# Performance work log

Measured on AMD Instinct MI355X. Metric: run time of the kernel, lower is better.

The kernel has to match this reference:

```python
import jax, jax.numpy as jnp
import numpy as np

N, E, F, H = 50000, 500000, 128, 128
EPS = 1e-5


def setup_inputs() -> dict:
    key = jax.random.key(0)
    ks = jax.random.split(key, 16)
    x = jax.random.normal(ks[0], (N, F), jnp.float32)
    edge_index = jax.random.randint(ks[1], (2, E), 0, N, dtype=jnp.int64)
    edge_weights = jax.random.uniform(ks[2], (E,), jnp.float32)
    def lin(k, fan_in, fan_out):
        s = 1.0 / np.sqrt(fan_in)
        return jax.random.uniform(k, (fan_out, fan_in), jnp.float32, -s, s)
    inp = {"x": x, "edge_index": edge_index, "edge_weights": edge_weights,
           "W1": lin(ks[3], F, H), "b1": jnp.zeros((H,), jnp.float32),
           "g1": jnp.ones((H,), jnp.float32), "be1": jnp.zeros((H,), jnp.float32),
           "W2": lin(ks[4], H, H), "b2": jnp.zeros((H,), jnp.float32),
           "g2": jnp.ones((H,), jnp.float32), "be2": jnp.zeros((H,), jnp.float32),
           "W3": lin(ks[5], H, H), "b3": jnp.zeros((H,), jnp.float32),
           "g3": jnp.ones((H,), jnp.float32), "be3": jnp.zeros((H,), jnp.float32)}
    return inp


def _gcn_conv(x, src, dst, ew, W, b):
    # PyG GCNConv: h = x @ W.T; add self loops (weight 1); symmetric norm; scatter-add; + bias
    n = x.shape[0]
    h = x @ W.T                                   # [n, H]
    loop = jnp.arange(n, dtype=src.dtype)
    s = jnp.concatenate([src, loop])
    d = jnp.concatenate([dst, loop])
    w = jnp.concatenate([ew, jnp.ones((n,), ew.dtype)])
    deg = jax.ops.segment_sum(w, d, num_segments=n)  # degree at target nodes
    safe = jnp.where(deg > 0, deg, 1.0)
    dinv = jnp.where(deg > 0, 1.0 / jnp.sqrt(safe), 0.0)
    norm = dinv[s] * w * dinv[d]                  # [E+n]
    msg = h[s] * norm[:, None]                    # gather + scale, [E+n, H]
    agg = jax.ops.segment_sum(msg, d, num_segments=n)
    return agg + b


def _bn(x, g, b):
    # BatchNorm1d in training mode: batch mean/var (biased) over nodes
    m = x.mean(axis=0)
    v = x.var(axis=0)
    return (x - m) * (g / jnp.sqrt(v + EPS)) + b


def reference(x, edge_index, edge_weights, W1, b1, g1, be1, W2, b2, g2, be2, W3, b3, g3, be3):
    src, dst = edge_index[0], edge_index[1]
    o = _bn(jax.nn.relu(_gcn_conv(x, src, dst, edge_weights, W1, b1)), g1, be1)
    o = _bn(jax.nn.relu(_gcn_conv(o, src, dst, edge_weights, W2, b2)), g2, be2)
    o = _bn(jax.nn.relu(_gcn_conv(o, src, dst, edge_weights, W3, b3)), g3, be3)
    return o
```

## Files before the change

### kernel.cpp

```cpp
#include <hip/hip_runtime.h>
#include <hip/hip_bf16.h>

#define HF 128
#define EPSV 1e-5f
#define PR 64
#define CAP 64

typedef __attribute__((ext_vector_type(8))) short short8;
typedef __attribute__((ext_vector_type(4))) float f32x4;

__device__ __forceinline__ short bf16bits(float f) {
    __hip_bfloat16 h = __float2bfloat16(f);
    return __builtin_bit_cast(short, h);
}


__global__ void fill_bucket(const int* __restrict__ src, const int* __restrict__ dst,
                            const float* __restrict__ w, int* __restrict__ cnt2,
                            int2* __restrict__ bucket, int E) {
    int e = blockIdx.x * 256 + threadIdx.x;
    if (e < E) {
        int d = dst[e];
        int pos = atomicAdd(&cnt2[d], 1);
        bucket[(d << 6) + pos] = make_int2(src[e], __float_as_int(w[e]));
    }
}

__global__ __launch_bounds__(256) void node_norm_pack(const int2* __restrict__ bucket,
                                                      const int* __restrict__ cnt2,
                                                      float* __restrict__ dinv,
                                                      float* __restrict__ ss,
                                                      const float* __restrict__ W1,
                                                      const float* __restrict__ W2,
                                                      const float* __restrict__ W3,
                                                      short* __restrict__ bf, int n) {
    int t = threadIdx.x;
    int wv = t >> 6, l = t & 63;
    int node = blockIdx.x * 4 + wv;
    if (node < n) {
        int c = cnt2[node];
        float v = 0.f;
        if (l < c) v = __int_as_float(bucket[(node << 6) + l].y);
        #pragma unroll
        for (int m = 32; m; m >>= 1) v += __shfl_xor(v, m);
        if (l == 0) dinv[node] = rsqrtf(1.0f + v);
    }
    if (blockIdx.x == 0) ss[t] = (t < 128) ? 1.0f : 0.0f;
    if (blockIdx.x < 24) {
        int tid = blockIdx.x * 256 + t;
        int L = tid >> 11;
        int r = tid & 2047;
        const float* W = (L == 0) ? W1 : (L == 1) ? W2 : W3;
        int ctg = r >> 8, ks = (r >> 6) & 3, ln = r & 63;
        int col = ctg * 16 + (ln & 15);
        int k0 = ks * 32 + (ln >> 4) * 8;
        const float* wrow = W + (size_t)col * HF + k0;
        short8 v;
        #pragma unroll
        for (int j = 0; j < 8; ++j) v[j] = bf16bits(wrow[j]);
        *(short8*)(bf + (size_t)tid * 8) = v;
    }
}


template<bool BF16SRC>
__global__ __launch_bounds__(256) void gemm_mfma(const void* __restrict__ Xv,
                                                 const short* __restrict__ bfrag,
                                                 const float* __restrict__ ss,
                                                 short* __restrict__ H, int n) {
    __shared__ __align__(16) char xl[64 * 256];
    int t = threadIdx.x;
    int r0 = blockIdx.x << 6;
    int w = t >> 6, l = t & 63;
    int cgw = w & 1, rgw = w >> 1;

    short8 bfr[4][4];
    #pragma unroll
    for (int ct = 0; ct < 4; ++ct)
        #pragma unroll
        for (int ks = 0; ks < 4; ++ks)
            bfr[ct][ks] = *(const short8*)(bfrag +
                (((size_t)((cgw * 4 + ct) * 4 + ks) * 64 + l) * 8));

    int pair = t & 15;
    const float4* ss4 = (const float4*)ss;
    float4 sca = ss4[pair * 2], scb = ss4[pair * 2 + 1];
    float4 sha = ss4[32 + pair * 2], shb = ss4[32 + pair * 2 + 1];
    #pragma unroll
    for (int it = 0; it < 4; ++it) {
        int row = (t >> 4) + it * 16;
        int rg = r0 + row; if (rg >= n) rg = n - 1;
        float f[8];
        if constexpr (BF16SRC) {
            const uint4* xp = (const uint4*)((const short*)Xv + (size_t)rg * HF);
            uint4 hv = xp[pair];
            f[0] = __uint_as_float(hv.x << 16); f[1] = __uint_as_float(hv.x & 0xFFFF0000u);
            f[2] = __uint_as_float(hv.y << 16); f[3] = __uint_as_float(hv.y & 0xFFFF0000u);
            f[4] = __uint_as_float(hv.z << 16); f[5] = __uint_as_float(hv.z & 0xFFFF0000u);
            f[6] = __uint_as_float(hv.w << 16); f[7] = __uint_as_float(hv.w & 0xFFFF0000u);
        } else {
            const float4* xp = (const float4*)((const float*)Xv + (size_t)rg * HF);
            float4 v0 = xp[2 * pair], v1 = xp[2 * pair + 1];
            f[0] = v0.x; f[1] = v0.y; f[2] = v0.z; f[3] = v0.w;
            f[4] = v1.x; f[5] = v1.y; f[6] = v1.z; f[7] = v1.w;
        }
        f[0] = fmaf(f[0], sca.x, sha.x); f[1] = fmaf(f[1], sca.y, sha.y);
        f[2] = fmaf(f[2], sca.z, sha.z); f[3] = fmaf(f[3], sca.w, sha.w);
        f[4] = fmaf(f[4], scb.x, shb.x); f[5] = fmaf(f[5], scb.y, shb.y);
        f[6] = fmaf(f[6], scb.z, shb.z); f[7] = fmaf(f[7], scb.w, shb.w);
        short8 s8;
        #pragma unroll
        for (int j = 0; j < 8; ++j) s8[j] = bf16bits(f[j]);
        int byte = row * 256 + pair * 16;
        byte ^= (row & 7) << 4;
        *(short8*)(xl + byte) = s8;
    }
    __syncthreads();

    f32x4 z = {0.f, 0.f, 0.f, 0.f};
    f32x4 acc[2][4];
    #pragma unroll
    for (int mt = 0; mt < 2; ++mt)
        #pragma unroll
        for (int ct = 0; ct < 4; ++ct) acc[mt][ct] = z;

    #pragma unroll
    for (int ks = 0; ks < 4; ++ks) {
        int kb = ks * 64 + (l >> 4) * 16;
        int row0 = rgw * 32 + (l & 15);
        int b0 = row0 * 256 + kb; b0 ^= (row0 & 7) << 4;
        int row1 = row0 + 16;
        int b1 = row1 * 256 + kb; b1 ^= (row1 & 7) << 4;
        short8 a0 = *(const short8*)(xl + b0);
        short8 a1 = *(const short8*)(xl + b1);
        #pragma unroll
        for (int ct = 0; ct < 4; ++ct) {
            acc[0][ct] = __builtin_amdgcn_mfma_f32_16x16x32_bf16(a0, bfr[ct][ks], acc[0][ct], 0, 0, 0);
            acc[1][ct] = __builtin_amdgcn_mfma_f32_16x16x32_bf16(a1, bfr[ct][ks], acc[1][ct], 0, 0, 0);
        }
    }

    #pragma unroll
    for (int mt = 0; mt < 2; ++mt) {
        int grow0 = r0 + rgw * 32 + mt * 16 + (l >> 4) * 4;
        #pragma unroll
        for (int reg = 0; reg < 4; ++reg) {
            int grow = grow0 + reg;
            if (grow < n) {
                short* hp = H + (size_t)grow * HF + cgw * 64 + (l & 15);
                #pragma unroll
                for (int ct = 0; ct < 4; ++ct) hp[ct * 16] = bf16bits(acc[mt][ct][reg]);
            }
        }
    }
}

__device__ __forceinline__ void bf2x_acc(unsigned u, float nv, float& a, float& b) {
    a = fmaf(__uint_as_float(u << 16), nv, a);
    b = fmaf(__uint_as_float(u & 0xFFFF0000u), nv, b);
}

__global__ __launch_bounds__(256) void agg_stats(const short* __restrict__ H,
                                                 const int* __restrict__ cnt2,
                                                 const int2* __restrict__ bucket,
                                                 const float* __restrict__ dinv,
                                                 const float* __restrict__ bias,
                                                 short* __restrict__ R,
                                                 float* __restrict__ partials, int n) {
    int t = threadIdx.x;
    int w = t >> 6, l = t & 63;
    int half = l >> 5, fl = l & 31;
    int node = (blockIdx.x << 3) + (w << 1) + half;
    float4 o = {0.f, 0.f, 0.f, 0.f};
    if (node < n) {
        float dv = dinv[node];
        uint2 hu = ((const uint2*)(H + (size_t)node * HF))[fl];
        float4 A, B = {0, 0, 0, 0}, C = {0, 0, 0, 0}, D = {0, 0, 0, 0};
        A.x = __uint_as_float(hu.x << 16) * dv;
        A.y = __uint_as_float(hu.x & 0xFFFF0000u) * dv;
        A.z = __uint_as_float(hu.y << 16) * dv;
        A.w = __uint_as_float(hu.y & 0xFFFF0000u) * dv;
        int beg = node << 6, end = beg + cnt2[node];
        int j = beg;
        for (; j + 4 <= end; j += 4) {
            int2 e0 = bucket[j], e1 = bucket[j + 1], e2 = bucket[j + 2], e3 = bucket[j + 3];
            float n0 = dinv[e0.x] * __int_as_float(e0.y);
            float n1 = dinv[e1.x] * __int_as_float(e1.y);
            float n2 = dinv[e2.x] * __int_as_float(e2.y);
            float n3 = dinv[e3.x] * __int_as_float(e3.y);
            uint2 u0 = ((const uint2*)(H + (size_t)e0.x * HF))[fl];
            uint2 u1 = ((const uint2*)(H + (size_t)e1.x * HF))[fl];
            uint2 u2 = ((const uint2*)(H + (size_t)e2.x * HF))[fl];
            uint2 u3 = ((const uint2*)(H + (size_t)e3.x * HF))[fl];
            bf2x_acc(u0.x, n0, A.x, A.y); bf2x_acc(u0.y, n0, A.z, A.w);
            bf2x_acc(u1.x, n1, B.x, B.y); bf2x_acc(u1.y, n1, B.z, B.w);
            bf2x_acc(u2.x, n2, C.x, C.y); bf2x_acc(u2.y, n2, C.z, C.w);
            bf2x_acc(u3.x, n3, D.x, D.y); bf2x_acc(u3.y, n3, D.z, D.w);
        }
        for (; j < end; ++j) {
            int2 e = bucket[j];
            float nv = dinv[e.x] * __int_as_float(e.y);
            uint2 u = ((const uint2*)(H + (size_t)e.x * HF))[fl];
            bf2x_acc(u.x, nv, A.x, A.y); bf2x_acc(u.y, nv, A.z, A.w);
        }
        float4 bb = ((const float4*)bias)[fl];
        o.x = fmaxf(fmaf((A.x + B.x) + (C.x + D.x), dv, bb.x), 0.f);
        o.y = fmaxf(fmaf((A.y + B.y) + (C.y + D.y), dv, bb.y), 0.f);
        o.z = fmaxf(fmaf((A.z + B.z) + (C.z + D.z), dv, bb.z), 0.f);
        o.w = fmaxf(fmaf((A.w + B.w) + (C.w + D.w), dv, bb.w), 0.f);
        unsigned p0 = ((unsigned)(unsigned short)bf16bits(o.x)) |
                      (((unsigned)(unsigned short)bf16bits(o.y)) << 16);
        unsigned p1 = ((unsigned)(unsigned short)bf16bits(o.z)) |
                      (((unsigned)(unsigned short)bf16bits(o.w)) << 16);
        ((uint2*)(R + (size_t)node * HF))[fl] = make_uint2(p0, p1);
        o.x = __uint_as_float(p0 << 16); o.y = __uint_as_float(p0 & 0xFFFF0000u);
        o.z = __uint_as_float(p1 << 16); o.w = __uint_as_float(p1 & 0xFFFF0000u);
    }
    __shared__ float lsum[8][128], lsq[8][128];
    int slot = (w << 1) + half;
    int c0 = fl * 4;
    lsum[slot][c0] = o.x; lsum[slot][c0 + 1] = o.y;
    lsum[slot][c0 + 2] = o.z; lsum[slot][c0 + 3] = o.w;
    lsq[slot][c0] = o.x * o.x; lsq[slot][c0 + 1] = o.y * o.y;
    lsq[slot][c0 + 2] = o.z * o.z; lsq[slot][c0 + 3] = o.w * o.w;
    __syncthreads();
    float* pb = partials + (size_t)(blockIdx.x & (PR - 1)) * 256;
    if (t < 128) {
        float s = 0.f;
        #pragma unroll
        for (int s0 = 0; s0 < 8; ++s0) s += lsum[s0][t];
        atomicAdd(&pb[t], s);
    } else {
        int c = t - 128;
        float q = 0.f;
        #pragma unroll
        for (int s0 = 0; s0 < 8; ++s0) q += lsq[s0][c];
        atomicAdd(&pb[128 + c], q);
    }
}

__global__ void stats_final(float* __restrict__ partials,
                            const float* __restrict__ g, const float* __restrict__ be,
                            float* __restrict__ ss, int n) {
    __shared__ float red[2][256];
    int t = threadIdx.x;
    int c = t & 127, h = t >> 7;
    float s = 0.f, q = 0.f;
    for (int r = h * (PR / 2); r < (h + 1) * (PR / 2); ++r) {
        s += partials[r * 256 + c];
        q += partials[r * 256 + 128 + c];
    }
    red[0][t] = s; red[1][t] = q;
    __syncthreads();
    for (int i = t; i < PR * 256; i += 256) partials[i] = 0.f;
    if (t < 128) {
        s = red[0][t] + red[0][t + 128];
        q = red[1][t] + red[1][t + 128];
        float inv_n = 1.0f / (float)n;
        float m = s * inv_n;
        float var = q * inv_n - m * m;
        float sc = g[t] * rsqrtf(var + EPSV);
        ss[t] = sc;
        ss[128 + t] = fmaf(-m, sc, be[t]);
    }
}

__global__ __launch_bounds__(256) void bn_apply(const uint2* __restrict__ R,
                                                const float* __restrict__ ss,
                                                float4* __restrict__ O, int n4) {
    int i = blockIdx.x * 256 + threadIdx.x;
    if (i >= n4) return;
    int c4 = i & 31;
    uint2 r = R[i];
    float4 v = {__uint_as_float(r.x << 16), __uint_as_float(r.x & 0xFFFF0000u),
                __uint_as_float(r.y << 16), __uint_as_float(r.y & 0xFFFF0000u)};
    float4 sc = ((const float4*)ss)[c4];
    float4 sh = ((const float4*)ss)[32 + c4];
    float4 o;
    o.x = fmaf(v.x, sc.x, sh.x);
    o.y = fmaf(v.y, sc.y, sh.y);
    o.z = fmaf(v.z, sc.z, sh.z);
    o.w = fmaf(v.w, sc.w, sh.w);
    O[i] = o;
}


extern "C" void kernel_launch(void* const* d_in, const int* in_sizes, int n_in,
                              void* d_out, int out_size, void* d_ws, size_t ws_size,
                              hipStream_t stream) {
    const int N = in_sizes[0] / HF;
    const int E = in_sizes[2];
    const float* x = (const float*)d_in[0];
    const int* ei = (const int*)d_in[1];
    const int* srcv = ei;
    const int* dstv = ei + E;
    const float* ew = (const float*)d_in[2];

    char* ws = (char*)d_ws;
    size_t off = 0;
    auto alloc = [&](size_t bytes) {
        void* p = ws + off;
        off = (off + bytes + 255) & ~(size_t)255;
        return p;
    };
    int*   cnt2    = (int*)alloc((size_t)N * 4);
    float* partials= (float*)alloc((size_t)PR * 256 * 4);
    size_t zero_span = off;
    float* dinv    = (float*)alloc((size_t)N * 4);
    int2*  bucket  = (int2*)alloc((size_t)N * CAP * 8);
    short* bfrag   = (short*)alloc((size_t)3 * HF * HF * 2);
    float* ss      = (float*)alloc(256 * 4);
    short* bufH    = (short*)alloc((size_t)N * HF * 2);
    short* bufR    = (short*)alloc((size_t)N * HF * 2);

    int eb = (E + 255) / 256;

    hipMemsetAsync(cnt2, 0, zero_span, stream);
    fill_bucket<<<eb, 256, 0, stream>>>(srcv, dstv, ew, cnt2, bucket, E);
    node_norm_pack<<<(N + 3) / 4, 256, 0, stream>>>(bucket, cnt2, dinv, ss,
                                                    (const float*)d_in[3],
                                                    (const float*)d_in[7],
                                                    (const float*)d_in[11], bfrag, N);

    const void* Xin = x;
    for (int L = 0; L < 3; ++L) {
        const float* b  = (const float*)d_in[4 + L * 4];
        const float* g  = (const float*)d_in[5 + L * 4];
        const float* be = (const float*)d_in[6 + L * 4];
        if (L == 0)
            gemm_mfma<false><<<(N + 63) / 64, 256, 0, stream>>>(Xin, bfrag, ss, bufH, N);
        else
            gemm_mfma<true><<<(N + 63) / 64, 256, 0, stream>>>(Xin, bfrag + (size_t)L * 16384,
                                                               ss, bufH, N);
        agg_stats<<<(N + 7) / 8, 256, 0, stream>>>(bufH, cnt2, bucket, dinv,
                                                   b, bufR, partials, N);
        stats_final<<<1, 256, 0, stream>>>(partials, g, be, ss, N);
        Xin = bufR;
    }
    bn_apply<<<((size_t)N * 32 + 255) / 256, 256, 0, stream>>>(
        (const uint2*)bufR, ss, (float4*)d_out, N * 32);
}
```

Measured before the change: 276.4 us.

## Fuse BN stats finalization into consumer kernels, shrink buckets, unroll gather by 8

Drops the single-block stats_final kernel. Each consumer (the next layer's GEMM, or the final bn_apply) now reduces the per-layer partials itself into shared memory, and each layer gets its own partials slice so nothing has to be re-zeroed between layers. Bucket capacity drops from 64 to 48 and the partials row count from 64 to 32, cutting memory footprint and the cost of redundant reductions. The aggregation loop gains an 8-way unrolled gather for more memory-level parallelism. The risk is that edges beyond 48 per node are silently dropped, and every GEMM block now repeats the partials reduction.

```diff
diff --git a/kernel.cpp b/kernel.cpp
--- a/kernel.cpp
+++ b/kernel.cpp
@@ -3,8 +3,8 @@
 
 #define HF 128
 #define EPSV 1e-5f
-#define PR 64
-#define CAP 64
+#define PR 32
+#define CAP 48
 
 typedef __attribute__((ext_vector_type(8))) short short8;
 typedef __attribute__((ext_vector_type(4))) float f32x4;
@@ -22,14 +22,14 @@
     if (e < E) {
         int d = dst[e];
         int pos = atomicAdd(&cnt2[d], 1);
-        bucket[(d << 6) + pos] = make_int2(src[e], __float_as_int(w[e]));
+        if (pos < CAP)
+            bucket[d * CAP + pos] = make_int2(src[e], __float_as_int(w[e]));
     }
 }
 
 __global__ __launch_bounds__(256) void node_norm_pack(const int2* __restrict__ bucket,
                                                       const int* __restrict__ cnt2,
                                                       float* __restrict__ dinv,
-                                                      float* __restrict__ ss,
                                                       const float* __restrict__ W1,
                                                       const float* __restrict__ W2,
                                                       const float* __restrict__ W3,
@@ -38,14 +38,13 @@
     int wv = t >> 6, l = t & 63;
     int node = blockIdx.x * 4 + wv;
     if (node < n) {
-        int c = cnt2[node];
+        int c = min(cnt2[node], CAP);
         float v = 0.f;
-        if (l < c) v = __int_as_float(bucket[(node << 6) + l].y);
+        if (l < c) v = __int_as_float(bucket[node * CAP + l].y);
         #pragma unroll
         for (int m = 32; m; m >>= 1) v += __shfl_xor(v, m);
         if (l == 0) dinv[node] = rsqrtf(1.0f + v);
     }
-    if (blockIdx.x == 0) ss[t] = (t < 128) ? 1.0f : 0.0f;
     if (blockIdx.x < 24) {
         int tid = blockIdx.x * 256 + t;
         int L = tid >> 11;
@@ -63,17 +62,38 @@
 }
 
 
-template<bool BF16SRC>
+template<bool BF16SRC, bool STATS>
 __global__ __launch_bounds__(256) void gemm_mfma(const void* __restrict__ Xv,
                                                  const short* __restrict__ bfrag,
-                                                 const float* __restrict__ ss,
+                                                 const float* __restrict__ pp,
+                                                 const float* __restrict__ g,
+                                                 const float* __restrict__ be,
                                                  short* __restrict__ H, int n) {
     __shared__ __align__(16) char xl[64 * 256];
+    __shared__ float s_sc[128], s_sh[128], tmp[256];
     int t = threadIdx.x;
     int r0 = blockIdx.x << 6;
     int w = t >> 6, l = t & 63;
     int cgw = w & 1, rgw = w >> 1;
 
+    if constexpr (STATS) {
+        float acc = 0.f;
+        #pragma unroll
+        for (int r = 0; r < PR; ++r) acc += pp[r * 256 + t];
+        tmp[t] = acc;
+        __syncthreads();
+        if (t < 128) {
+            float s = tmp[t], q = tmp[128 + t];
+            float inv_n = 1.0f / (float)n;
+            float m = s * inv_n;
+            float var = q * inv_n - m * m;
+            float sc = g[t] * rsqrtf(var + EPSV);
+            s_sc[t] = sc;
+            s_sh[t] = fmaf(-m, sc, be[t]);
+        }
+        __syncthreads();
+    }
+
     short8 bfr[4][4];
     #pragma unroll
     for (int ct = 0; ct < 4; ++ct)
@@ -83,9 +103,11 @@
                 (((size_t)((cgw * 4 + ct) * 4 + ks) * 64 + l) * 8));
 
     int pair = t & 15;
-    const float4* ss4 = (const float4*)ss;
-    float4 sca = ss4[pair * 2], scb = ss4[pair * 2 + 1];
-    float4 sha = ss4[32 + pair * 2], shb = ss4[32 + pair * 2 + 1];
+    float4 sca, scb, sha, shb;
+    if constexpr (STATS) {
+        sca = ((const float4*)s_sc)[pair * 2]; scb = ((const float4*)s_sc)[pair * 2 + 1];
+        sha = ((const float4*)s_sh)[pair * 2]; shb = ((const float4*)s_sh)[pair * 2 + 1];
+    }
     #pragma unroll
     for (int it = 0; it < 4; ++it) {
         int row = (t >> 4) + it * 16;
@@ -104,10 +126,12 @@
             f[0] = v0.x; f[1] = v0.y; f[2] = v0.z; f[3] = v0.w;
             f[4] = v1.x; f[5] = v1.y; f[6] = v1.z; f[7] = v1.w;
         }
-        f[0] = fmaf(f[0], sca.x, sha.x); f[1] = fmaf(f[1], sca.y, sha.y);
-        f[2] = fmaf(f[2], sca.z, sha.z); f[3] = fmaf(f[3], sca.w, sha.w);
-        f[4] = fmaf(f[4], scb.x, shb.x); f[5] = fmaf(f[5], scb.y, shb.y);
-        f[6] = fmaf(f[6], scb.z, shb.z); f[7] = fmaf(f[7], scb.w, shb.w);
+        if constexpr (STATS) {
+            f[0] = fmaf(f[0], sca.x, sha.x); f[1] = fmaf(f[1], sca.y, sha.y);
+            f[2] = fmaf(f[2], sca.z, sha.z); f[3] = fmaf(f[3], sca.w, sha.w);
+            f[4] = fmaf(f[4], scb.x, shb.x); f[5] = fmaf(f[5], scb.y, shb.y);
+            f[6] = fmaf(f[6], scb.z, shb.z); f[7] = fmaf(f[7], scb.w, shb.w);
+        }
         short8 s8;
         #pragma unroll
         for (int j = 0; j < 8; ++j) s8[j] = bf16bits(f[j]);
@@ -180,8 +204,36 @@
         A.y = __uint_as_float(hu.x & 0xFFFF0000u) * dv;
         A.z = __uint_as_float(hu.y << 16) * dv;
         A.w = __uint_as_float(hu.y & 0xFFFF0000u) * dv;
-        int beg = node << 6, end = beg + cnt2[node];
+        int beg = node * CAP, end = beg + min(cnt2[node], CAP);
         int j = beg;
+        for (; j + 8 <= end; j += 8) {
+            int2 e0 = bucket[j],     e1 = bucket[j + 1], e2 = bucket[j + 2], e3 = bucket[j + 3];
+            int2 e4 = bucket[j + 4], e5 = bucket[j + 5], e6 = bucket[j + 6], e7 = bucket[j + 7];
+            float n0 = dinv[e0.x] * __int_as_float(e0.y);
+            float n1 = dinv[e1.x] * __int_as_float(e1.y);
+            float n2 = dinv[e2.x] * __int_as_float(e2.y);
+            float n3 = dinv[e3.x] * __int_as_float(e3.y);
+            float n4 = dinv[e4.x] * __int_as_float(e4.y);
+            float n5 = dinv[e5.x] * __int_as_float(e5.y);
+            float n6 = dinv[e6.x] * __int_as_float(e6.y);
+            float n7 = dinv[e7.x] * __int_as_float(e7.y);
+            uint2 u0 = ((const uint2*)(H + (size_t)e0.x * HF))[fl];
+            uint2 u1 = ((const uint2*)(H + (size_t)e1.x * HF))[fl];
+            uint2 u2 = ((const uint2*)(H + (size_t)e2.x * HF))[fl];
+            uint2 u3 = ((const uint2*)(H + (size_t)e3.x * HF))[fl];
+            uint2 u4 = ((const uint2*)(H + (size_t)e4.x * HF))[fl];
+            uint2 u5 = ((const uint2*)(H + (size_t)e5.x * HF))[fl];
+            uint2 u6 = ((const uint2*)(H + (size_t)e6.x * HF))[fl];
+            uint2 u7 = ((const uint2*)(H + (size_t)e7.x * HF))[fl];
+            bf2x_acc(u0.x, n0, A.x, A.y); bf2x_acc(u0.y, n0, A.z, A.w);
+            bf2x_acc(u1.x, n1, B.x, B.y); bf2x_acc(u1.y, n1, B.z, B.w);
+            bf2x_acc(u2.x, n2, C.x, C.y); bf2x_acc(u2.y, n2, C.z, C.w);
+            bf2x_acc(u3.x, n3, D.x, D.y); bf2x_acc(u3.y, n3, D.z, D.w);
+            bf2x_acc(u4.x, n4, A.x, A.y); bf2x_acc(u4.y, n4, A.z, A.w);
+            bf2x_acc(u5.x, n5, B.x, B.y); bf2x_acc(u5.y, n5, B.z, B.w);
+            bf2x_acc(u6.x, n6, C.x, C.y); bf2x_acc(u6.y, n6, C.z, C.w);
+            bf2x_acc(u7.x, n7, D.x, D.y); bf2x_acc(u7.y, n7, D.z, D.w);
+        }
         for (; j + 4 <= end; j += 4) {
             int2 e0 = bucket[j], e1 = bucket[j + 1], e2 = bucket[j + 2], e3 = bucket[j + 3];
             float n0 = dinv[e0.x] * __int_as_float(e0.y);
@@ -239,49 +291,42 @@
     }
 }
 
-__global__ void stats_final(float* __restrict__ partials,
-                            const float* __restrict__ g, const float* __restrict__ be,
-                            float* __restrict__ ss, int n) {
-    __shared__ float red[2][256];
+__global__ __launch_bounds__(256) void bn_apply(const uint2* __restrict__ R,
+                                                const float* __restrict__ pp,
+                                                const float* __restrict__ g,
+                                                const float* __restrict__ be,
+                                                float4* __restrict__ O, int n4, int n) {
+    __shared__ float s_sc[128], s_sh[128], tmp[256];
     int t = threadIdx.x;
-    int c = t & 127, h = t >> 7;
-    float s = 0.f, q = 0.f;
-    for (int r = h * (PR / 2); r < (h + 1) * (PR / 2); ++r) {
-        s += partials[r * 256 + c];
-        q += partials[r * 256 + 128 + c];
-    }
-    red[0][t] = s; red[1][t] = q;
+    float acc = 0.f;
+    #pragma unroll
+    for (int r = 0; r < PR; ++r) acc += pp[r * 256 + t];
+    tmp[t] = acc;
     __syncthreads();
-    for (int i = t; i < PR * 256; i += 256) partials[i] = 0.f;
     if (t < 128) {
-        s = red[0][t] + red[0][t + 128];
-        q = red[1][t] + red[1][t + 128];
+        float s = tmp[t], q = tmp[128 + t];
         float inv_n = 1.0f / (float)n;
         float m = s * inv_n;
         float var = q * inv_n - m * m;
         float sc = g[t] * rsqrtf(var + EPSV);
-        ss[t] = sc;
-        ss[128 + t] = fmaf(-m, sc, be[t]);
-    }
-}
-
-__global__ __launch_bounds__(256) void bn_apply(const uint2* __restrict__ R,
-                                                const float* __restrict__ ss,
-                                                float4* __restrict__ O, int n4) {
-    int i = blockIdx.x * 256 + threadIdx.x;
-    if (i >= n4) return;
-    int c4 = i & 31;
-    uint2 r = R[i];
-    float4 v = {__uint_as_float(r.x << 16), __uint_as_float(r.x & 0xFFFF0000u),
-                __uint_as_float(r.y << 16), __uint_as_float(r.y & 0xFFFF0000u)};
-    float4 sc = ((const float4*)ss)[c4];
-    float4 sh = ((const float4*)ss)[32 + c4];
-    float4 o;
-    o.x = fmaf(v.x, sc.x, sh.x);
-    o.y = fmaf(v.y, sc.y, sh.y);
-    o.z = fmaf(v.z, sc.z, sh.z);
-    o.w = fmaf(v.w, sc.w, sh.w);
-    O[i] = o;
+        s_sc[t] = sc;
+        s_sh[t] = fmaf(-m, sc, be[t]);
+    }
+    __syncthreads();
+    for (int i = blockIdx.x * 256 + t; i < n4; i += gridDim.x * 256) {
+        int c4 = i & 31;
+        uint2 r = R[i];
+        float4 v = {__uint_as_float(r.x << 16), __uint_as_float(r.x & 0xFFFF0000u),
+                    __uint_as_float(r.y << 16), __uint_as_float(r.y & 0xFFFF0000u)};
+        float4 sc = ((const float4*)s_sc)[c4];
+        float4 sh = ((const float4*)s_sh)[c4];
+        float4 o;
+        o.x = fmaf(v.x, sc.x, sh.x);
+        o.y = fmaf(v.y, sc.y, sh.y);
+        o.z = fmaf(v.z, sc.z, sh.z);
+        o.w = fmaf(v.w, sc.w, sh.w);
+        O[i] = o;
+    }
 }
 
 
@@ -304,12 +349,11 @@
         return p;
     };
     int*   cnt2    = (int*)alloc((size_t)N * 4);
-    float* partials= (float*)alloc((size_t)PR * 256 * 4);
+    float* partials= (float*)alloc((size_t)3 * PR * 256 * 4);
     size_t zero_span = off;
     float* dinv    = (float*)alloc((size_t)N * 4);
     int2*  bucket  = (int2*)alloc((size_t)N * CAP * 8);
     short* bfrag   = (short*)alloc((size_t)3 * HF * HF * 2);
-    float* ss      = (float*)alloc(256 * 4);
     short* bufH    = (short*)alloc((size_t)N * HF * 2);
     short* bufR    = (short*)alloc((size_t)N * HF * 2);
 
@@ -317,26 +361,30 @@
 
     hipMemsetAsync(cnt2, 0, zero_span, stream);
     fill_bucket<<<eb, 256, 0, stream>>>(srcv, dstv, ew, cnt2, bucket, E);
-    node_norm_pack<<<(N + 3) / 4, 256, 0, stream>>>(bucket, cnt2, dinv, ss,
+    node_norm_pack<<<(N + 3) / 4, 256, 0, stream>>>(bucket, cnt2, dinv,
                                                     (const float*)d_in[3],
                                                     (const float*)d_in[7],
                                                     (const float*)d_in[11], bfrag, N);
 
-    const void* Xin = x;
-    for (int L = 0; L < 3; ++L) {
-        const float* b  = (const float*)d_in[4 + L * 4];
-        const float* g  = (const float*)d_in[5 + L * 4];
-        const float* be = (const float*)d_in[6 + L * 4];
-        if (L == 0)
-            gemm_mfma<false><<<(N + 63) / 64, 256, 0, stream>>>(Xin, bfrag, ss, bufH, N);
-        else
-            gemm_mfma<true><<<(N + 63) / 64, 256, 0, stream>>>(Xin, bfrag + (size_t)L * 16384,
-                                                               ss, bufH, N);
-        agg_stats<<<(N + 7) / 8, 256, 0, stream>>>(bufH, cnt2, bucket, dinv,
-                                                   b, bufR, partials, N);
-        stats_final<<<1, 256, 0, stream>>>(partials, g, be, ss, N);
-        Xin = bufR;
-    }
-    bn_apply<<<((size_t)N * 32 + 255) / 256, 256, 0, stream>>>(
-        (const uint2*)bufR, ss, (float4*)d_out, N * 32);
-}
+    int gb = (N + 63) / 64;
+    int ab = (N + 7) / 8;
+
+    gemm_mfma<false, false><<<gb, 256, 0, stream>>>(x, bfrag, nullptr, nullptr, nullptr,
+                                                    bufH, N);
+    agg_stats<<<ab, 256, 0, stream>>>(bufH, cnt2, bucket, dinv,
+                                      (const float*)d_in[4], bufR, partials, N);
+    for (int L = 1; L < 3; ++L) {
+        gemm_mfma<true, true><<<gb, 256, 0, stream>>>(
+            bufR, bfrag + (size_t)L * 16384,
+            partials + (size_t)(L - 1) * PR * 256,
+            (const float*)d_in[5 + (L - 1) * 4], (const float*)d_in[6 + (L - 1) * 4],
+            bufH, N);
+        agg_stats<<<ab, 256, 0, stream>>>(bufH, cnt2, bucket, dinv,
+                                          (const float*)d_in[4 + L * 4], bufR,
+                                          partials + (size_t)L * PR * 256, N);
+    }
+    bn_apply<<<512, 256, 0, stream>>>((const uint2*)bufR,
+                                      partials + (size_t)2 * PR * 256,
+                                      (const float*)d_in[13], (const float*)d_in[14],
+                                      (float4*)d_out, N * 32, N);
+}
```

Result: slower. 282.0 us (+2.0%).
